# Performance work log

Measured on AMD Instinct MI355X. Metric: run time of the kernel, lower is better.

## Reference

```python
import jax, jax.numpy as jnp
import numpy as np

STRIDES = (8.0, 16.0, 32.0)
REG_MAX = 7
TOP_K = 100          # top_k_n: max per class and max total
NMS_PRE = 1000       # hardcoded prefilter in get_bboxes
IOU_THRES = 0.5      # literal passed to combined_non_max_suppression
BOX_SCORE = 0.3
IMG_SIZE = (640.0, 640.0)


def _centers(h, w, stride):
    # row-major (h, w) flatten, points stored as (y, x)
    y = (jnp.arange(h, dtype=jnp.float32) + 0.5) * stride
    x = (jnp.arange(w, dtype=jnp.float32) + 0.5) * stride
    return jnp.stack([jnp.repeat(y, w), jnp.tile(x, h)], axis=-1)  # [h*w, 2]


def _distribution(bbox_pred, stride):
    # softmax over reg_max+1 bins -> expected distance, scaled by stride
    b = bbox_pred.shape[0]
    p = jax.nn.softmax(bbox_pred.reshape(b, -1, REG_MAX + 1), axis=-1)
    ln = jnp.arange(REG_MAX + 1, dtype=jnp.float32)
    d = jnp.einsum('bnk,k->bn', p, ln).reshape(b, -1, 4)
    return d * stride


def _process_level(cls_score, bbox_pred, stride):
    b, h, w, c = cls_score.shape
    scores = jax.nn.sigmoid(cls_score.reshape(b, h * w, c))
    dist = _distribution(bbox_pred, stride)                     # [b, hw, 4]
    pts = jnp.broadcast_to(_centers(h, w, stride)[None], (b, h * w, 2))
    if h * w > NMS_PRE:  # static shape check, mirrors TF graph specialization
        max_scores = jnp.max(scores, axis=-1)                   # [b, hw]
        _, topk = jax.lax.top_k(max_scores, NMS_PRE)            # [b, NMS_PRE]
        scores = jnp.take_along_axis(scores, topk[..., None], axis=1)
        dist = jnp.take_along_axis(dist, topk[..., None], axis=1)
        pts = jnp.take_along_axis(pts, topk[..., None], axis=1)
    # distance2bbox with clipping to model input shape
    y1 = jnp.clip(pts[..., 0] - dist[..., 0], 0.0, IMG_SIZE[0])
    x1 = jnp.clip(pts[..., 1] - dist[..., 1], 0.0, IMG_SIZE[1])
    y2 = jnp.clip(pts[..., 0] + dist[..., 2], 0.0, IMG_SIZE[0])
    x2 = jnp.clip(pts[..., 1] + dist[..., 3], 0.0, IMG_SIZE[1])
    return jnp.stack([y1, x1, y2, x2], axis=-1), scores


def _iou_1_vs_n(box, boxes):
    yy1 = jnp.maximum(box[0], boxes[:, 0])
    xx1 = jnp.maximum(box[1], boxes[:, 1])
    yy2 = jnp.minimum(box[2], boxes[:, 2])
    xx2 = jnp.minimum(box[3], boxes[:, 3])
    inter = jnp.maximum(yy2 - yy1, 0.0) * jnp.maximum(xx2 - xx1, 0.0)
    a1 = (box[2] - box[0]) * (box[3] - box[1])
    a2 = (boxes[:, 2] - boxes[:, 0]) * (boxes[:, 3] - boxes[:, 1])
    return inter / (a1 + a2 - inter + 1e-9)


def _nms_single(boxes, scores):
    # greedy NMS, fixed TOP_K iterations; boxes [N,4], scores [N]
    def step(s, _):
        i = jnp.argmax(s)
        sc = s[i]
        suppress = _iou_1_vs_n(boxes[i], boxes) > IOU_THRES
        s = jnp.where(suppress, -jnp.inf, s)
        s = s.at[i].set(-jnp.inf)
        return s, (i, sc)
    _, (idx, sel) = jax.lax.scan(step, scores, None, length=TOP_K)
    return idx, sel  # [TOP_K] each


def _combined_nms(boxes, scores):
    # per-class NMS then global top-K, emulating tf.image.combined_non_max_suppression
    n, c = scores.shape
    idx, sel = jax.vmap(_nms_single, in_axes=(None, 1))(boxes, scores)  # [C, K]
    sel_boxes = boxes[idx]                                              # [C, K, 4]
    cls = jnp.broadcast_to(jnp.arange(c, dtype=jnp.float32)[:, None], (c, TOP_K))
    flat_s = sel.reshape(-1)
    flat_s = jnp.where(jnp.isfinite(flat_s), flat_s, -1.0)
    top_s, top_i = jax.lax.top_k(flat_s, TOP_K)
    out_boxes = sel_boxes.reshape(-1, 4)[top_i]
    out_cls = cls.reshape(-1)[top_i]
    ok = top_s > -1.0
    out_s = jnp.where(ok, top_s, 0.0)
    out_boxes = jnp.where(ok[:, None], out_boxes, 0.0)
    out_cls = jnp.where(ok, out_cls, 0.0)
    return out_boxes, out_s, out_cls


def setup_inputs() -> dict:
    key = jax.random.key(0)
    ks = jax.random.split(key, 7)
    b, c = 16, 20
    inp = {}
    for i, hw in enumerate((80, 40, 20)):
        inp[f'cls_score_{i}'] = jax.random.normal(ks[i], (b, hw, hw, c), dtype=jnp.float32)
        inp[f'bbox_pred_{i}'] = jax.random.normal(ks[3 + i], (b, hw, hw, 4 * (REG_MAX + 1)), dtype=jnp.float32)
    inp['origin_shapes'] = jax.random.uniform(ks[6], (b, 2), dtype=jnp.float32) * 1280.0
    return inp


def reference(cls_score_0, cls_score_1, cls_score_2,
              bbox_pred_0, bbox_pred_1, bbox_pred_2, origin_shapes):
    cls_scores = (cls_score_0, cls_score_1, cls_score_2)
    bbox_preds = (bbox_pred_0, bbox_pred_1, bbox_pred_2)
    mlvl_b, mlvl_s = [], []
    for cs, bp, st in zip(cls_scores, bbox_preds, STRIDES):
        bb, sc = _process_level(cs, bp, st)
        mlvl_b.append(bb)
        mlvl_s.append(sc)
    boxes = jnp.concatenate(mlvl_b, axis=1)    # [B, 2400, 4]
    scores = jnp.concatenate(mlvl_s, axis=1)   # [B, 2400, C]
    nb, ns, nc = jax.vmap(_combined_nms)(boxes, scores)
    out = jnp.concatenate([nb, ns[..., None], nc[..., None]], axis=-1)  # [B, K, 6]
    mask = (ns > BOX_SCORE).astype(out.dtype)
    return out * mask[..., None]
```

## Files before the change

### kernel.cpp

```cpp
#include <hip/hip_runtime.h>
#include <math.h>

#define BATCH 16
#define NCLS 20
#define TOPK 100
#define NPRE 1000
#define NTOT 2400
#define NBINS 8
#define N0 6400
#define N1 1600
#define SSEL 256

#define MID05 0.50000002980232238769531250

__device__ __forceinline__ unsigned int orderable(float x) {
    unsigned int u = __float_as_uint(x);
    return (u & 0x80000000u) ? ~u : (u | 0x80000000u);
}
__device__ __forceinline__ float unorderable(unsigned int k) {
    return __uint_as_float((k & 0x80000000u) ? (k ^ 0x80000000u) : ~k);
}

__device__ __forceinline__ void radix_pass_scan(
        const unsigned int* hist, unsigned int* s_prefix, unsigned int* s_kk,
        unsigned int prefix, unsigned int kk, int t) {
    if (t < 64) {
        uint4 h = *(const uint4*)&hist[t * 4];
        unsigned int s3 = h.w;
        unsigned int s2 = h.z + s3;
        unsigned int s1 = h.y + s2;
        unsigned int s0 = h.x + s1;
        unsigned int S = s0;
        #pragma unroll
        for (int off = 1; off < 64; off <<= 1) {
            unsigned int o = __shfl_down(S, off);
            S += (t + off < 64) ? o : 0u;
        }
        unsigned int Sgt = S - s0;
        unsigned int F0 = s0 + Sgt, F1 = s1 + Sgt, F2 = s2 + Sgt, F3 = s3 + Sgt;
        if (F0 >= kk && F1 < kk)  { *s_prefix = (prefix << 8) | (unsigned int)(t * 4 + 0); *s_kk = kk - F1; }
        if (F1 >= kk && F2 < kk)  { *s_prefix = (prefix << 8) | (unsigned int)(t * 4 + 1); *s_kk = kk - F2; }
        if (F2 >= kk && F3 < kk)  { *s_prefix = (prefix << 8) | (unsigned int)(t * 4 + 2); *s_kk = kk - F3; }
        if (F3 >= kk && Sgt < kk) { *s_prefix = (prefix << 8) | (unsigned int)(t * 4 + 3); *s_kk = kk - Sgt; }
    }
}

__device__ __forceinline__ unsigned long long bmerge_shfl(
        unsigned long long v, int t, int k2, int jmax) {
    for (int j2 = jmax; j2 > 0; j2 >>= 1) {
        unsigned long long o = __shfl_xor(v, j2);
        bool km = (((t & k2) == 0) == ((t & j2) != 0));
        v = km ? (v > o ? v : o) : (v < o ? v : o);
    }
    return v;
}

__global__ __launch_bounds__(1024) void select_keys_kernel(
        const float* __restrict__ cls0, const float* __restrict__ cls1,
        int* __restrict__ sel_idx, int* __restrict__ cnt) {
    int bid = blockIdx.x;
    int b = bid >> 1;
    int lvl = bid & 1;
    int n = (lvl == 0) ? N0 : N1;
    const float* cls = (lvl == 0 ? cls0 : cls1) + (size_t)b * (size_t)n * NCLS;

    __shared__ unsigned int skey[N0];
    __shared__ __align__(16) unsigned int hist[256];
    __shared__ int eq[256];
    __shared__ unsigned int s_prefix, s_kk, s_cnt, s_eqcnt;
    int t = threadIdx.x;

    if (bid == 0 && t < BATCH) cnt[t] = 0;

    for (int a = t; a < n; a += 1024) {
        const float4* p4 = (const float4*)(cls + (size_t)a * NCLS);
        float m = -INFINITY;
        #pragma unroll
        for (int q = 0; q < 5; ++q) {
            float4 v = p4[q];
            m = fmaxf(m, fmaxf(fmaxf(v.x, v.y), fmaxf(v.z, v.w)));
        }
        skey[a] = orderable(m);
    }
    if (t == 0) { s_kk = NPRE; s_prefix = 0u; s_cnt = 0u; s_eqcnt = 0u; }
    __syncthreads();

    for (int pass = 0; pass < 4; ++pass) {
        int shift = 24 - 8 * pass;
        unsigned int prefix = s_prefix, kk = s_kk;
        if (t < 256) hist[t] = 0u;
        __syncthreads();
        for (int a = t; a < n; a += 1024) {
            unsigned int u = skey[a];
            if (pass == 0 || (u >> (shift + 8)) == prefix)
                atomicAdd(&hist[(u >> shift) & 255u], 1u);
        }
        __syncthreads();
        radix_pass_scan(hist, &s_prefix, &s_kk, prefix, kk, t);
        __syncthreads();
    }

    unsigned int T = s_prefix;
    int* out = sel_idx + b * 2000 + lvl * 1000;
    for (int a = t; a < n; a += 1024) {
        unsigned int u = skey[a];
        if (u > T) {
            unsigned int pos = atomicAdd(&s_cnt, 1u);
            out[pos] = a;
        } else if (u == T) {
            unsigned int p = atomicAdd(&s_eqcnt, 1u);
            if (p < 256u) eq[p] = a;
        }
    }
    __syncthreads();
    if (t == 0) {
        unsigned int pos = s_cnt;
        unsigned int rem = s_kk;
        unsigned int cnt2 = s_eqcnt;
        if (cnt2 <= 256u) {
            for (unsigned int i = 1; i < cnt2; ++i) {
                int key = eq[i]; int j2 = (int)i - 1;
                while (j2 >= 0 && eq[j2] > key) { eq[j2 + 1] = eq[j2]; --j2; }
                eq[j2 + 1] = key;
            }
            for (unsigned int i = 0; i < rem; ++i) out[pos + i] = eq[i];
        } else {
            for (int a = 0; a < n && rem > 0u; ++a)
                if (skey[a] == T) { out[pos++] = a; --rem; }
        }
    }
}

__global__ __launch_bounds__(256) void decode_kernel(
        const float* __restrict__ cls0, const float* __restrict__ cls1, const float* __restrict__ cls2,
        const float* __restrict__ bb0,  const float* __restrict__ bb1,  const float* __restrict__ bb2,
        const int* __restrict__ sel_idx,
        float* __restrict__ boxes_all, float* __restrict__ scores_t) {
    int tg = blockIdx.x * blockDim.x + threadIdx.x;
    if (tg >= BATCH * NTOT) return;
    int b = tg / NTOT, j = tg % NTOT;

    const float* cls; const float* bb; int a, w; float stride;
    if (j < 1000) {
        a = sel_idx[b * 2000 + j]; w = 80; stride = 8.f;
        cls = cls0 + ((size_t)b * N0 + a) * NCLS;
        bb  = bb0  + ((size_t)b * N0 + a) * 32;
    } else if (j < 2000) {
        a = sel_idx[b * 2000 + j]; w = 40; stride = 16.f;
        cls = cls1 + ((size_t)b * N1 + a) * NCLS;
        bb  = bb1  + ((size_t)b * N1 + a) * 32;
    } else {
        a = j - 2000; w = 20; stride = 32.f;
        cls = cls2 + ((size_t)b * 400 + a) * NCLS;
        bb  = bb2  + ((size_t)b * 400 + a) * 32;
    }

    float cl[20];
    {
        const float4* c4 = (const float4*)cls;
        #pragma unroll
        for (int q = 0; q < 5; ++q) *(float4*)&cl[q * 4] = c4[q];
    }
    float bl[32];
    {
        const float4* b4 = (const float4*)bb;
        #pragma unroll
        for (int q = 0; q < 8; ++q) *(float4*)&bl[q * 4] = b4[q];
    }

    #pragma unroll
    for (int c = 0; c < NCLS; ++c)
        scores_t[((size_t)b * NCLS + c) * NTOT + j] = 1.f / (1.f + expf(-cl[c]));

    float d[4];
    #pragma unroll
    for (int s = 0; s < 4; ++s) {
        const float* l = &bl[s * NBINS];
        float m = l[0];
        #pragma unroll
        for (int k = 1; k < NBINS; ++k) m = fmaxf(m, l[k]);
        float e[NBINS], sum = 0.f;
        #pragma unroll
        for (int k = 0; k < NBINS; ++k) { e[k] = expf(l[k] - m); sum += e[k]; }
        float acc = 0.f;
        #pragma unroll
        for (int k = 0; k < NBINS; ++k) acc += (e[k] / sum) * (float)k;
        d[s] = acc * stride;
    }
    float cy = ((float)(a / w) + 0.5f) * stride;
    float cx = ((float)(a % w) + 0.5f) * stride;
    float* bx = boxes_all + ((size_t)b * NTOT + j) * 4;
    bx[0] = fminf(fmaxf(cy - d[0], 0.f), 640.f);
    bx[1] = fminf(fmaxf(cx - d[1], 0.f), 640.f);
    bx[2] = fminf(fmaxf(cy + d[2], 0.f), 640.f);
    bx[3] = fminf(fmaxf(cx + d[3], 0.f), 640.f);
}

__global__ __launch_bounds__(256) void class_nms_kernel(
        const float* __restrict__ boxes_all, const float* __restrict__ scores_t,
        float* __restrict__ nms_score, int* __restrict__ nms_idx,
        int* __restrict__ cnt, float* __restrict__ outbuf) {
    int blk = blockIdx.x;
    int b = blk / NCLS;
    int t = threadIdx.x;

    __shared__ unsigned int skey[NTOT];
    __shared__ __align__(16) unsigned int hist[256];
    __shared__ int eq[128];
    __shared__ unsigned int s_prefix, s_kk, s_cnt, s_eqcnt;
    __shared__ unsigned long long sorted[SSEL];
    __shared__ float4 abox[TOPK];
    __shared__ float4 cbox[64];
    __shared__ int s_outPos;
    __shared__ unsigned long long s_m;
    __shared__ int s_last;

    const float*  ssrc = scores_t + (size_t)blk * NTOT;
    const float4* bsrc = (const float4*)boxes_all + (size_t)b * NTOT;
    float* osc = nms_score + (size_t)blk * TOPK;
    int*   oid = nms_idx   + (size_t)blk * TOPK;

    for (int j = t; j < NTOT; j += 256) skey[j] = orderable(ssrc[j]);
    if (t == 0) { s_kk = SSEL; s_prefix = 0u; s_cnt = 0u; s_eqcnt = 0u; s_outPos = 0; }
    __syncthreads();

    for (int pass = 0; pass < 4; ++pass) {
        int shift = 24 - 8 * pass;
        unsigned int prefix = s_prefix, kk = s_kk;
        hist[t] = 0u;
        __syncthreads();
        for (int j = t; j < NTOT; j += 256) {
            unsigned int u = skey[j];
            if (pass == 0 || (u >> (shift + 8)) == prefix)
                atomicAdd(&hist[(u >> shift) & 255u], 1u);
        }
        __syncthreads();
        radix_pass_scan(hist, &s_prefix, &s_kk, prefix, kk, t);
        __syncthreads();
    }

    unsigned int T = s_prefix;
    for (int j = t; j < NTOT; j += 256) {
        unsigned int u = skey[j];
        if (u > T) {
            unsigned int pos = atomicAdd(&s_cnt, 1u);
            sorted[pos] = ((unsigned long long)u << 32) | (unsigned int)~j;
        } else if (u == T) {
            unsigned int p = atomicAdd(&s_eqcnt, 1u);
            if (p < 128u) eq[p] = j;
        }
    }
    __syncthreads();
    if (t == 0) {
        unsigned int pos = s_cnt;
        unsigned int rem = s_kk;
        unsigned int cnt2 = s_eqcnt;
        if (cnt2 <= 128u) {
            for (unsigned int i = 1; i < cnt2; ++i) {
                int key = eq[i]; int j2 = (int)i - 1;
                while (j2 >= 0 && eq[j2] > key) { eq[j2 + 1] = eq[j2]; --j2; }
                eq[j2 + 1] = key;
            }
            for (unsigned int i = 0; i < rem; ++i)
                sorted[pos + i] = ((unsigned long long)T << 32) | (unsigned int)~eq[i];
        } else {
            for (int j = 0; j < NTOT && rem > 0u; ++j)
                if (skey[j] == T) {
                    sorted[pos++] = ((unsigned long long)T << 32) | (unsigned int)~j;
                    --rem;
                }
        }
    }
    __syncthreads();

    {
        unsigned long long v = sorted[t];
        #pragma unroll
        for (int k2 = 2; k2 <= 64; k2 <<= 1)
            v = bmerge_shfl(v, t, k2, k2 >> 1);
        sorted[t] = v;
        __syncthreads();
        {
            unsigned long long o = sorted[t ^ 64];
            bool km = (((t & 128) == 0) == ((t & 64) != 0));
            v = km ? (v > o ? v : o) : (v < o ? v : o);
            v = bmerge_shfl(v, t, 128, 32);
        }
        __syncthreads();
        sorted[t] = v;
        __syncthreads();
        {
            unsigned long long o = sorted[t ^ 128];
            bool km = ((t & 128) != 0);
            v = km ? (v > o ? v : o) : (v < o ? v : o);
        }
        __syncthreads();
        sorted[t] = v;
        __syncthreads();
        {
            unsigned long long o = sorted[t ^ 64];
            bool km = ((t & 64) != 0);
            v = km ? (v > o ? v : o) : (v < o ? v : o);
            v = bmerge_shfl(v, t, 256, 32);
        }
        __syncthreads();
        sorted[t] = v;
        __syncthreads();
    }

    if (t < 64) {
        int lane = t;
        int outPos = 0;
        for (int chunk = 0; chunk < SSEL / 64 && outPos < TOPK; ++chunk) {
            unsigned long long key = sorted[SSEL - 1 - (chunk * 64 + lane)];
            unsigned int j = ~(unsigned int)key;
            float sc = unorderable((unsigned int)(key >> 32));
            float4 bj = bsrc[j];
            cbox[lane] = bj;
            float amine = (bj.z - bj.x) * (bj.w - bj.y);

            bool sup = false;
            for (int t2 = 0; t2 < outPos; ++t2) {
                float4 wb = abox[t2];
                float a1 = (wb.z - wb.x) * (wb.w - wb.y);
                float yy1 = fmaxf(wb.x, bj.x);
                float xx1 = fmaxf(wb.y, bj.y);
                float yy2 = fminf(wb.z, bj.z);
                float xx2 = fminf(wb.w, bj.w);
                float inter = fmaxf(yy2 - yy1, 0.f) * fmaxf(xx2 - xx1, 0.f);
                float denom = a1 + amine - inter + 1e-9f;
                sup = sup || ((double)inter > MID05 * (double)denom);
            }

            unsigned long long supmask = 0ull;
            #pragma unroll 8
            for (int j2 = 0; j2 < 64; ++j2) {
                float4 wb = cbox[j2];
                float a1 = (wb.z - wb.x) * (wb.w - wb.y);
                float yy1 = fmaxf(wb.x, bj.x);
                float xx1 = fmaxf(wb.y, bj.y);
                float yy2 = fminf(wb.z, bj.z);
                float xx2 = fminf(wb.w, bj.w);
                float inter = fmaxf(yy2 - yy1, 0.f) * fmaxf(xx2 - xx1, 0.f);
                float denom = a1 + amine - inter + 1e-9f;
                bool s2 = ((double)inter > MID05 * (double)denom);
                if (s2 && j2 < lane) supmask |= (1ull << j2);
            }

            unsigned long long cand = __ballot(!sup);
            unsigned long long accbits = 0ull;
            while (cand) {
                int i = __builtin_ctzll(cand);
                accbits |= (1ull << i);
                cand &= ~(1ull << i);
                unsigned long long row = __ballot((supmask >> i) & 1ull);
                cand &= ~row;
            }

            int nAcc = (int)__builtin_popcountll(accbits);
            int avail = TOPK - outPos;
            bool mine = (accbits >> lane) & 1ull;
            int myrank = (int)__builtin_popcountll(accbits & ((1ull << lane) - 1ull));
            if (mine && myrank < avail) {
                int pos = outPos + myrank;
                osc[pos] = sc;
                oid[pos] = (int)j;
                abox[pos] = bj;
            }
            outPos += (nAcc < avail) ? nAcc : avail;
            __builtin_amdgcn_s_waitcnt(0);
        }
        if (lane == 0) s_outPos = outPos;
    }
    __syncthreads();

    int outPos = s_outPos;
    if (outPos < TOPK) {
        if (t < SSEL) skey[~(unsigned int)sorted[t]] = 0u;
        __syncthreads();
        for (int j = t; j < NTOT; j += 256) {
            unsigned int u = skey[j];
            if (!u) continue;
            float4 bj = bsrc[j];
            float amine = (bj.z - bj.x) * (bj.w - bj.y);
            bool sup = false;
            for (int t2 = 0; t2 < outPos; ++t2) {
                float4 wb = abox[t2];
                float a1 = (wb.z - wb.x) * (wb.w - wb.y);
                float yy1 = fmaxf(wb.x, bj.x);
                float xx1 = fmaxf(wb.y, bj.y);
                float yy2 = fminf(wb.z, bj.z);
                float xx2 = fminf(wb.w, bj.w);
                float inter = fmaxf(yy2 - yy1, 0.f) * fmaxf(xx2 - xx1, 0.f);
                float denom = a1 + amine - inter + 1e-9f;
                sup = sup || ((double)inter > MID05 * (double)denom);
            }
            if (sup) skey[j] = 0u;
        }
        __syncthreads();
        while (outPos < TOPK) {
            if (t == 0) s_m = 0ull;
            __syncthreads();
            unsigned long long loc = 0ull;
            for (int j = t; j < NTOT; j += 256) {
                unsigned int u = skey[j];
                if (u) {
                    unsigned long long kk = ((unsigned long long)u << 32) | (unsigned int)~j;
                    loc = (kk > loc) ? kk : loc;
                }
            }
            atomicMax(&s_m, loc);
            __syncthreads();
            unsigned long long m = s_m;
            if ((long long)m >= 0) break;
            unsigned int wi = ~(unsigned int)m;
            float4 wb = bsrc[wi];
            if (t == 0) {
                osc[outPos] = unorderable((unsigned int)(m >> 32));
                oid[outPos] = (int)wi;
                skey[wi] = 0u;
            }
            __syncthreads();
            float a1 = (wb.z - wb.x) * (wb.w - wb.y);
            for (int j = t; j < NTOT; j += 256) {
                unsigned int u = skey[j];
                if (!u) continue;
                float4 bj = bsrc[j];
                float yy1 = fmaxf(wb.x, bj.x);
                float xx1 = fmaxf(wb.y, bj.y);
                float yy2 = fminf(wb.z, bj.z);
                float xx2 = fminf(wb.w, bj.w);
                float inter = fmaxf(yy2 - yy1, 0.f) * fmaxf(xx2 - xx1, 0.f);
                float a2 = (bj.z - bj.x) * (bj.w - bj.y);
                float denom = a1 + a2 - inter + 1e-9f;
                if ((double)inter > MID05 * (double)denom) skey[j] = 0u;
            }
            ++outPos;
            __syncthreads();
        }
    }

    for (int k2 = outPos + t; k2 < TOPK; k2 += 256) { osc[k2] = -INFINITY; oid[k2] = 0; }

    __syncthreads();
    if (t == 0) {
        __threadfence();
        int old = atomicAdd(&cnt[b], 1);
        s_last = (old == NCLS - 1) ? 1 : 0;
        if (s_last) __threadfence();
    }
    __syncthreads();
    if (!s_last) return;

    for (int f = t; f < 2000; f += 256) {
        float s = nms_score[(size_t)b * 2000 + f];
        float v = isfinite(s) ? s : -1.0f;
        skey[f] = orderable(v);
    }
    if (t == 0) { s_kk = TOPK; s_prefix = 0u; s_cnt = 0u; s_eqcnt = 0u; }
    if (t < 128) sorted[t] = 0ull;
    __syncthreads();

    for (int pass = 0; pass < 4; ++pass) {
        int shift = 24 - 8 * pass;
        unsigned int prefix = s_prefix, kk = s_kk;
        hist[t] = 0u;
        __syncthreads();
        for (int f = t; f < 2000; f += 256) {
            unsigned int u = skey[f];
            if (pass == 0 || (u >> (shift + 8)) == prefix)
                atomicAdd(&hist[(u >> shift) & 255u], 1u);
        }
        __syncthreads();
        radix_pass_scan(hist, &s_prefix, &s_kk, prefix, kk, t);
        __syncthreads();
    }

    unsigned int Tf = s_prefix;
    for (int f = t; f < 2000; f += 256) {
        unsigned int u = skey[f];
        if (u > Tf) {
            unsigned int pos = atomicAdd(&s_cnt, 1u);
            sorted[pos] = ((unsigned long long)u << 32) | (unsigned int)~f;
        } else if (u == Tf) {
            unsigned int p = atomicAdd(&s_eqcnt, 1u);
            if (p < 128u) eq[p] = f;
        }
    }
    __syncthreads();
    if (t == 0) {
        unsigned int pos = s_cnt;
        unsigned int rem = s_kk;
        unsigned int cnt2 = s_eqcnt;
        if (cnt2 <= 128u) {
            for (unsigned int i = 1; i < cnt2; ++i) {
                int key = eq[i]; int j2 = (int)i - 1;
                while (j2 >= 0 && eq[j2] > key) { eq[j2 + 1] = eq[j2]; --j2; }
                eq[j2 + 1] = key;
            }
            for (unsigned int i = 0; i < rem; ++i)
                sorted[pos + i] = ((unsigned long long)Tf << 32) | (unsigned int)~eq[i];
        } else {
            for (int f = 0; f < 2000 && rem > 0u; ++f)
                if (skey[f] == Tf) {
                    sorted[pos++] = ((unsigned long long)Tf << 32) | (unsigned int)~f;
                    --rem;
                }
        }
    }
    __syncthreads();

    {
        unsigned long long v = (t < 128) ? sorted[t] : 0ull;
        if (t < 128) {
            #pragma unroll
            for (int k2 = 2; k2 <= 64; k2 <<= 1)
                v = bmerge_shfl(v, t, k2, k2 >> 1);
            sorted[t] = v;
        }
        __syncthreads();
        if (t < 128) {
            unsigned long long o = sorted[t ^ 64];
            bool km = ((t & 64) != 0);
            v = km ? (v > o ? v : o) : (v < o ? v : o);
            v = bmerge_shfl(v, t, 128, 32);
        }
        __syncthreads();
        if (t < 128) sorted[t] = v;
        __syncthreads();
    }

    if (t < TOPK) {
        unsigned long long kk = sorted[127 - t];
        float v = unorderable((unsigned int)(kk >> 32));
        int fi = (int)~(unsigned int)kk;
        float* o = outbuf + ((size_t)b * TOPK + t) * 6;
        if (v > 0.3f) {
            int bidx = nms_idx[(size_t)b * 2000 + fi];
            float4 bxw = ((const float4*)boxes_all)[(size_t)b * NTOT + bidx];
            o[0] = bxw.x; o[1] = bxw.y; o[2] = bxw.z; o[3] = bxw.w;
            o[4] = v; o[5] = (float)(fi / TOPK);
        } else {
            o[0] = 0.f; o[1] = 0.f; o[2] = 0.f; o[3] = 0.f; o[4] = 0.f; o[5] = 0.f;
        }
    }
}

extern "C" void kernel_launch(void* const* d_in, const int* in_sizes, int n_in,
                              void* d_out, int out_size, void* d_ws, size_t ws_size,
                              hipStream_t stream) {
    (void)out_size; (void)ws_size;
    const float* cls[3] = {nullptr, nullptr, nullptr};
    const float* bbx[3] = {nullptr, nullptr, nullptr};
    for (int i = 0; i < n_in; ++i) {
        const float* p = (const float*)d_in[i];
        switch (in_sizes[i]) {
            case 16 * 6400 * 20: cls[0] = p; break;
            case 16 * 6400 * 32: bbx[0] = p; break;
            case 16 * 1600 * 20: cls[1] = p; break;
            case 16 * 1600 * 32: bbx[1] = p; break;
            case 16 *  400 * 20: cls[2] = p; break;
            case 16 *  400 * 32: bbx[2] = p; break;
            default: break;
        }
    }

    char* w = (char*)d_ws;
    int*   sel_idx    = (int*)(w);
    float* boxes_all  = (float*)(w + 131072);
    float* scores_t   = (float*)(w + 745472);
    float* nms_score  = (float*)(w + 3817472);
    int*   nms_idx    = (int*)(w + 3945472);
    int*   cnt        = (int*)(w + 4073472);

    hipLaunchKernelGGL(select_keys_kernel, dim3(32), dim3(1024), 0, stream,
                       cls[0], cls[1], sel_idx, cnt);
    hipLaunchKernelGGL(decode_kernel, dim3((BATCH * NTOT + 255) / 256), dim3(256), 0, stream,
                       cls[0], cls[1], cls[2], bbx[0], bbx[1], bbx[2],
                       sel_idx, boxes_all, scores_t);
    hipLaunchKernelGGL(class_nms_kernel, dim3(BATCH * NCLS), dim3(256), 0, stream,
                       boxes_all, scores_t, nms_score, nms_idx, cnt, (float*)d_out);
}
```

Before: 154.2 us.

## Split key computation into wide kernel and pair two classes per NMS block

The per-anchor max-score key computation moves out of the 32-block select kernel into a separate fully parallel kernel, and the radix select then reads precomputed keys with 256 threads. The class NMS kernel now processes two classes per 512-thread block, which halves the block count and the final-merge counter threshold. The aim is to remove the low-parallelism prologue of select and to amortize the final per-batch merge across fewer blocks. The cost is an extra launch, a global round-trip for the keys, and more shared memory per NMS block, which may reduce occupancy. The fallback NMS loop for classes that do not finish within the sorted prefix now runs serially over both classes using the whole block.

```diff
diff --git a/kernel.cpp b/kernel.cpp
--- a/kernel.cpp
+++ b/kernel.cpp
@@ -23,46 +23,71 @@
 
 __device__ __forceinline__ void radix_pass_scan(
         const unsigned int* hist, unsigned int* s_prefix, unsigned int* s_kk,
-        unsigned int prefix, unsigned int kk, int t) {
-    if (t < 64) {
-        uint4 h = *(const uint4*)&hist[t * 4];
-        unsigned int s3 = h.w;
-        unsigned int s2 = h.z + s3;
-        unsigned int s1 = h.y + s2;
-        unsigned int s0 = h.x + s1;
-        unsigned int S = s0;
-        #pragma unroll
-        for (int off = 1; off < 64; off <<= 1) {
-            unsigned int o = __shfl_down(S, off);
-            S += (t + off < 64) ? o : 0u;
-        }
-        unsigned int Sgt = S - s0;
-        unsigned int F0 = s0 + Sgt, F1 = s1 + Sgt, F2 = s2 + Sgt, F3 = s3 + Sgt;
-        if (F0 >= kk && F1 < kk)  { *s_prefix = (prefix << 8) | (unsigned int)(t * 4 + 0); *s_kk = kk - F1; }
-        if (F1 >= kk && F2 < kk)  { *s_prefix = (prefix << 8) | (unsigned int)(t * 4 + 1); *s_kk = kk - F2; }
-        if (F2 >= kk && F3 < kk)  { *s_prefix = (prefix << 8) | (unsigned int)(t * 4 + 2); *s_kk = kk - F3; }
-        if (F3 >= kk && Sgt < kk) { *s_prefix = (prefix << 8) | (unsigned int)(t * 4 + 3); *s_kk = kk - Sgt; }
-    }
+        unsigned int prefix, unsigned int kk, int lane) {
+    uint4 h = *(const uint4*)&hist[lane * 4];
+    unsigned int s3 = h.w;
+    unsigned int s2 = h.z + s3;
+    unsigned int s1 = h.y + s2;
+    unsigned int s0 = h.x + s1;
+    unsigned int S = s0;
+    #pragma unroll
+    for (int off = 1; off < 64; off <<= 1) {
+        unsigned int o = __shfl_down(S, off);
+        S += (lane + off < 64) ? o : 0u;
+    }
+    unsigned int Sgt = S - s0;
+    unsigned int F0 = s0 + Sgt, F1 = s1 + Sgt, F2 = s2 + Sgt, F3 = s3 + Sgt;
+    if (F0 >= kk && F1 < kk)  { *s_prefix = (prefix << 8) | (unsigned int)(lane * 4 + 0); *s_kk = kk - F1; }
+    if (F1 >= kk && F2 < kk)  { *s_prefix = (prefix << 8) | (unsigned int)(lane * 4 + 1); *s_kk = kk - F2; }
+    if (F2 >= kk && F3 < kk)  { *s_prefix = (prefix << 8) | (unsigned int)(lane * 4 + 2); *s_kk = kk - F3; }
+    if (F3 >= kk && Sgt < kk) { *s_prefix = (prefix << 8) | (unsigned int)(lane * 4 + 3); *s_kk = kk - Sgt; }
 }
 
 __device__ __forceinline__ unsigned long long bmerge_shfl(
-        unsigned long long v, int t, int k2, int jmax) {
+        unsigned long long v, int pos, int k2, int jmax) {
     for (int j2 = jmax; j2 > 0; j2 >>= 1) {
         unsigned long long o = __shfl_xor(v, j2);
-        bool km = (((t & k2) == 0) == ((t & j2) != 0));
+        bool km = (((pos & k2) == 0) == ((pos & j2) != 0));
         v = km ? (v > o ? v : o) : (v < o ? v : o);
     }
     return v;
 }
 
-__global__ __launch_bounds__(1024) void select_keys_kernel(
+__global__ __launch_bounds__(256) void compute_keys_kernel(
         const float* __restrict__ cls0, const float* __restrict__ cls1,
-        int* __restrict__ sel_idx, int* __restrict__ cnt) {
+        unsigned int* __restrict__ keys0, unsigned int* __restrict__ keys1,
+        int* __restrict__ cnt) {
+    int tg = blockIdx.x * 256 + threadIdx.x;
+    if (blockIdx.x == 0 && threadIdx.x < BATCH) cnt[threadIdx.x] = 0;
+    const float* p;
+    unsigned int* dst;
+    if (tg < BATCH * N0) {
+        p = cls0 + (size_t)tg * NCLS;
+        dst = keys0 + tg;
+    } else {
+        int a = tg - BATCH * N0;
+        if (a >= BATCH * N1) return;
+        p = cls1 + (size_t)a * NCLS;
+        dst = keys1 + a;
+    }
+    const float4* p4 = (const float4*)p;
+    float m = -INFINITY;
+    #pragma unroll
+    for (int q = 0; q < 5; ++q) {
+        float4 v = p4[q];
+        m = fmaxf(m, fmaxf(fmaxf(v.x, v.y), fmaxf(v.z, v.w)));
+    }
+    *dst = orderable(m);
+}
+
+__global__ __launch_bounds__(256) void radix_select_kernel(
+        const unsigned int* __restrict__ keys0, const unsigned int* __restrict__ keys1,
+        int* __restrict__ sel_idx) {
     int bid = blockIdx.x;
     int b = bid >> 1;
     int lvl = bid & 1;
     int n = (lvl == 0) ? N0 : N1;
-    const float* cls = (lvl == 0 ? cls0 : cls1) + (size_t)b * (size_t)n * NCLS;
+    const unsigned int* gk = (lvl == 0 ? keys0 : keys1) + (size_t)b * n;
 
     __shared__ unsigned int skey[N0];
     __shared__ __align__(16) unsigned int hist[256];
@@ -70,39 +95,28 @@
     __shared__ unsigned int s_prefix, s_kk, s_cnt, s_eqcnt;
     int t = threadIdx.x;
 
-    if (bid == 0 && t < BATCH) cnt[t] = 0;
-
-    for (int a = t; a < n; a += 1024) {
-        const float4* p4 = (const float4*)(cls + (size_t)a * NCLS);
-        float m = -INFINITY;
-        #pragma unroll
-        for (int q = 0; q < 5; ++q) {
-            float4 v = p4[q];
-            m = fmaxf(m, fmaxf(fmaxf(v.x, v.y), fmaxf(v.z, v.w)));
-        }
-        skey[a] = orderable(m);
-    }
+    for (int a = t; a < n; a += 256) skey[a] = gk[a];
     if (t == 0) { s_kk = NPRE; s_prefix = 0u; s_cnt = 0u; s_eqcnt = 0u; }
     __syncthreads();
 
     for (int pass = 0; pass < 4; ++pass) {
         int shift = 24 - 8 * pass;
         unsigned int prefix = s_prefix, kk = s_kk;
-        if (t < 256) hist[t] = 0u;
-        __syncthreads();
-        for (int a = t; a < n; a += 1024) {
+        hist[t] = 0u;
+        __syncthreads();
+        for (int a = t; a < n; a += 256) {
             unsigned int u = skey[a];
             if (pass == 0 || (u >> (shift + 8)) == prefix)
                 atomicAdd(&hist[(u >> shift) & 255u], 1u);
         }
         __syncthreads();
-        radix_pass_scan(hist, &s_prefix, &s_kk, prefix, kk, t);
+        if (t < 64) radix_pass_scan(hist, &s_prefix, &s_kk, prefix, kk, t);
         __syncthreads();
     }
 
     unsigned int T = s_prefix;
     int* out = sel_idx + b * 2000 + lvl * 1000;
-    for (int a = t; a < n; a += 1024) {
+    for (int a = t; a < n; a += 256) {
         unsigned int u = skey[a];
         if (u > T) {
             unsigned int pos = atomicAdd(&s_cnt, 1u);
@@ -196,77 +210,82 @@
     bx[3] = fminf(fmaxf(cx + d[3], 0.f), 640.f);
 }
 
-__global__ __launch_bounds__(256) void class_nms_kernel(
+__global__ __launch_bounds__(512) void class_nms_kernel(
         const float* __restrict__ boxes_all, const float* __restrict__ scores_t,
         float* __restrict__ nms_score, int* __restrict__ nms_idx,
         int* __restrict__ cnt, float* __restrict__ outbuf) {
     int blk = blockIdx.x;
-    int b = blk / NCLS;
+    int b = blk / 10;
+    int pair = blk % 10;
     int t = threadIdx.x;
-
-    __shared__ unsigned int skey[NTOT];
-    __shared__ __align__(16) unsigned int hist[256];
-    __shared__ int eq[128];
-    __shared__ unsigned int s_prefix, s_kk, s_cnt, s_eqcnt;
-    __shared__ unsigned long long sorted[SSEL];
-    __shared__ float4 abox[TOPK];
-    __shared__ float4 cbox[64];
-    __shared__ int s_outPos;
-    __shared__ unsigned long long s_m;
+    int ci = t >> 8;
+    int tl = t & 255;
+    int c = pair * 2 + ci;
+
+    __shared__ unsigned int skey[2][NTOT];
+    __shared__ __align__(16) unsigned int hist[2][256];
+    __shared__ int eq[2][128];
+    __shared__ unsigned int s_prefix[2], s_kk[2], s_cnt[2], s_eqcnt[2];
+    __shared__ unsigned long long sorted[2][SSEL];
+    __shared__ float4 abox[2][TOPK];
+    __shared__ float4 cbox[2][64];
+    __shared__ int s_outPos[2];
+    __shared__ unsigned long long s_m[2];
     __shared__ int s_last;
 
-    const float*  ssrc = scores_t + (size_t)blk * NTOT;
+    const float*  ssrc = scores_t + ((size_t)b * NCLS + c) * NTOT;
     const float4* bsrc = (const float4*)boxes_all + (size_t)b * NTOT;
-    float* osc = nms_score + (size_t)blk * TOPK;
-    int*   oid = nms_idx   + (size_t)blk * TOPK;
-
-    for (int j = t; j < NTOT; j += 256) skey[j] = orderable(ssrc[j]);
-    if (t == 0) { s_kk = SSEL; s_prefix = 0u; s_cnt = 0u; s_eqcnt = 0u; s_outPos = 0; }
+    float* osc = nms_score + ((size_t)b * NCLS + c) * TOPK;
+    int*   oid = nms_idx   + ((size_t)b * NCLS + c) * TOPK;
+
+    for (int j = tl; j < NTOT; j += 256) skey[ci][j] = orderable(ssrc[j]);
+    if (tl == 0) { s_kk[ci] = SSEL; s_prefix[ci] = 0u; s_cnt[ci] = 0u; s_eqcnt[ci] = 0u; s_outPos[ci] = 0; }
     __syncthreads();
 
     for (int pass = 0; pass < 4; ++pass) {
         int shift = 24 - 8 * pass;
-        unsigned int prefix = s_prefix, kk = s_kk;
-        hist[t] = 0u;
-        __syncthreads();
-        for (int j = t; j < NTOT; j += 256) {
-            unsigned int u = skey[j];
+        unsigned int prefix = s_prefix[ci], kk = s_kk[ci];
+        hist[ci][tl] = 0u;
+        __syncthreads();
+        for (int j = tl; j < NTOT; j += 256) {
+            unsigned int u = skey[ci][j];
             if (pass == 0 || (u >> (shift + 8)) == prefix)
-                atomicAdd(&hist[(u >> shift) & 255u], 1u);
-        }
-        __syncthreads();
-        radix_pass_scan(hist, &s_prefix, &s_kk, prefix, kk, t);
-        __syncthreads();
-    }
-
-    unsigned int T = s_prefix;
-    for (int j = t; j < NTOT; j += 256) {
-        unsigned int u = skey[j];
+                atomicAdd(&hist[ci][(u >> shift) & 255u], 1u);
+        }
+        __syncthreads();
+        if (tl < 64)
+            radix_pass_scan(hist[ci], &s_prefix[ci], &s_kk[ci], prefix, kk, tl);
+        __syncthreads();
+    }
+
+    unsigned int T = s_prefix[ci];
+    for (int j = tl; j < NTOT; j += 256) {
+        unsigned int u = skey[ci][j];
         if (u > T) {
-            unsigned int pos = atomicAdd(&s_cnt, 1u);
-            sorted[pos] = ((unsigned long long)u << 32) | (unsigned int)~j;
+            unsigned int pos = atomicAdd(&s_cnt[ci], 1u);
+            sorted[ci][pos] = ((unsigned long long)u << 32) | (unsigned int)~j;
         } else if (u == T) {
-            unsigned int p = atomicAdd(&s_eqcnt, 1u);
-            if (p < 128u) eq[p] = j;
-        }
-    }
-    __syncthreads();
-    if (t == 0) {
-        unsigned int pos = s_cnt;
-        unsigned int rem = s_kk;
-        unsigned int cnt2 = s_eqcnt;
+            unsigned int p = atomicAdd(&s_eqcnt[ci], 1u);
+            if (p < 128u) eq[ci][p] = j;
+        }
+    }
+    __syncthreads();
+    if (tl == 0) {
+        unsigned int pos = s_cnt[ci];
+        unsigned int rem = s_kk[ci];
+        unsigned int cnt2 = s_eqcnt[ci];
         if (cnt2 <= 128u) {
             for (unsigned int i = 1; i < cnt2; ++i) {
-                int key = eq[i]; int j2 = (int)i - 1;
-                while (j2 >= 0 && eq[j2] > key) { eq[j2 + 1] = eq[j2]; --j2; }
-                eq[j2 + 1] = key;
+                int key = eq[ci][i]; int j2 = (int)i - 1;
+                while (j2 >= 0 && eq[ci][j2] > key) { eq[ci][j2 + 1] = eq[ci][j2]; --j2; }
+                eq[ci][j2 + 1] = key;
             }
             for (unsigned int i = 0; i < rem; ++i)
-                sorted[pos + i] = ((unsigned long long)T << 32) | (unsigned int)~eq[i];
+                sorted[ci][pos + i] = ((unsigned long long)T << 32) | (unsigned int)~eq[ci][i];
         } else {
             for (int j = 0; j < NTOT && rem > 0u; ++j)
-                if (skey[j] == T) {
-                    sorted[pos++] = ((unsigned long long)T << 32) | (unsigned int)~j;
+                if (skey[ci][j] == T) {
+                    sorted[ci][pos++] = ((unsigned long long)T << 32) | (unsigned int)~j;
                     --rem;
                 }
         }
@@ -274,54 +293,54 @@
     __syncthreads();
 
     {
-        unsigned long long v = sorted[t];
+        unsigned long long v = sorted[ci][tl];
         #pragma unroll
         for (int k2 = 2; k2 <= 64; k2 <<= 1)
-            v = bmerge_shfl(v, t, k2, k2 >> 1);
-        sorted[t] = v;
+            v = bmerge_shfl(v, tl, k2, k2 >> 1);
+        sorted[ci][tl] = v;
         __syncthreads();
         {
-            unsigned long long o = sorted[t ^ 64];
-            bool km = (((t & 128) == 0) == ((t & 64) != 0));
+            unsigned long long o = sorted[ci][tl ^ 64];
+            bool km = (((tl & 128) == 0) == ((tl & 64) != 0));
             v = km ? (v > o ? v : o) : (v < o ? v : o);
-            v = bmerge_shfl(v, t, 128, 32);
-        }
-        __syncthreads();
-        sorted[t] = v;
+            v = bmerge_shfl(v, tl, 128, 32);
+        }
+        __syncthreads();
+        sorted[ci][tl] = v;
         __syncthreads();
         {
-            unsigned long long o = sorted[t ^ 128];
-            bool km = ((t & 128) != 0);
+            unsigned long long o = sorted[ci][tl ^ 128];
+            bool km = ((tl & 128) != 0);
             v = km ? (v > o ? v : o) : (v < o ? v : o);
         }
         __syncthreads();
-        sorted[t] = v;
+        sorted[ci][tl] = v;
         __syncthreads();
         {
-            unsigned long long o = sorted[t ^ 64];
-            bool km = ((t & 64) != 0);
+            unsigned long long o = sorted[ci][tl ^ 64];
+            bool km = ((tl & 64) != 0);
             v = km ? (v > o ? v : o) : (v < o ? v : o);
-            v = bmerge_shfl(v, t, 256, 32);
-        }
-        __syncthreads();
-        sorted[t] = v;
-        __syncthreads();
-    }
-
-    if (t < 64) {
-        int lane = t;
+            v = bmerge_shfl(v, tl, 256, 32);
+        }
+        __syncthreads();
+        sorted[ci][tl] = v;
+        __syncthreads();
+    }
+
+    if (tl < 64) {
+        int lane = tl;
         int outPos = 0;
         for (int chunk = 0; chunk < SSEL / 64 && outPos < TOPK; ++chunk) {
-            unsigned long long key = sorted[SSEL - 1 - (chunk * 64 + lane)];
+            unsigned long long key = sorted[ci][SSEL - 1 - (chunk * 64 + lane)];
             unsigned int j = ~(unsigned int)key;
             float sc = unorderable((unsigned int)(key >> 32));
             float4 bj = bsrc[j];
-            cbox[lane] = bj;
+            cbox[ci][lane] = bj;
             float amine = (bj.z - bj.x) * (bj.w - bj.y);
 
             bool sup = false;
             for (int t2 = 0; t2 < outPos; ++t2) {
-                float4 wb = abox[t2];
+                float4 wb = abox[ci][t2];
                 float a1 = (wb.z - wb.x) * (wb.w - wb.y);
                 float yy1 = fmaxf(wb.x, bj.x);
                 float xx1 = fmaxf(wb.y, bj.y);
@@ -335,7 +354,7 @@
             unsigned long long supmask = 0ull;
             #pragma unroll 8
             for (int j2 = 0; j2 < 64; ++j2) {
-                float4 wb = cbox[j2];
+                float4 wb = cbox[ci][j2];
                 float a1 = (wb.z - wb.x) * (wb.w - wb.y);
                 float yy1 = fmaxf(wb.x, bj.x);
                 float xx1 = fmaxf(wb.y, bj.y);
@@ -365,145 +384,155 @@
                 int pos = outPos + myrank;
                 osc[pos] = sc;
                 oid[pos] = (int)j;
-                abox[pos] = bj;
+                abox[ci][pos] = bj;
             }
             outPos += (nAcc < avail) ? nAcc : avail;
             __builtin_amdgcn_s_waitcnt(0);
         }
-        if (lane == 0) s_outPos = outPos;
-    }
-    __syncthreads();
-
-    int outPos = s_outPos;
-    if (outPos < TOPK) {
-        if (t < SSEL) skey[~(unsigned int)sorted[t]] = 0u;
-        __syncthreads();
-        for (int j = t; j < NTOT; j += 256) {
-            unsigned int u = skey[j];
-            if (!u) continue;
-            float4 bj = bsrc[j];
-            float amine = (bj.z - bj.x) * (bj.w - bj.y);
-            bool sup = false;
-            for (int t2 = 0; t2 < outPos; ++t2) {
-                float4 wb = abox[t2];
-                float a1 = (wb.z - wb.x) * (wb.w - wb.y);
-                float yy1 = fmaxf(wb.x, bj.x);
-                float xx1 = fmaxf(wb.y, bj.y);
-                float yy2 = fminf(wb.z, bj.z);
-                float xx2 = fminf(wb.w, bj.w);
-                float inter = fmaxf(yy2 - yy1, 0.f) * fmaxf(xx2 - xx1, 0.f);
-                float denom = a1 + amine - inter + 1e-9f;
-                sup = sup || ((double)inter > MID05 * (double)denom);
-            }
-            if (sup) skey[j] = 0u;
-        }
-        __syncthreads();
-        while (outPos < TOPK) {
-            if (t == 0) s_m = 0ull;
+        if (lane == 0) s_outPos[ci] = outPos;
+    }
+    __syncthreads();
+
+    for (int ci2 = 0; ci2 < 2; ++ci2) {
+        int outPos = s_outPos[ci2];
+        if (outPos < TOPK) {
+            int c2 = pair * 2 + ci2;
+            float* osc2 = nms_score + ((size_t)b * NCLS + c2) * TOPK;
+            int*   oid2 = nms_idx   + ((size_t)b * NCLS + c2) * TOPK;
+            if (t < SSEL) skey[ci2][~(unsigned int)sorted[ci2][t]] = 0u;
             __syncthreads();
-            unsigned long long loc = 0ull;
-            for (int j = t; j < NTOT; j += 256) {
-                unsigned int u = skey[j];
-                if (u) {
-                    unsigned long long kk = ((unsigned long long)u << 32) | (unsigned int)~j;
-                    loc = (kk > loc) ? kk : loc;
-                }
-            }
-            atomicMax(&s_m, loc);
-            __syncthreads();
-            unsigned long long m = s_m;
-            if ((long long)m >= 0) break;
-            unsigned int wi = ~(unsigned int)m;
-            float4 wb = bsrc[wi];
-            if (t == 0) {
-                osc[outPos] = unorderable((unsigned int)(m >> 32));
-                oid[outPos] = (int)wi;
-                skey[wi] = 0u;
-            }
-            __syncthreads();
-            float a1 = (wb.z - wb.x) * (wb.w - wb.y);
-            for (int j = t; j < NTOT; j += 256) {
-                unsigned int u = skey[j];
+            for (int j = t; j < NTOT; j += 512) {
+                unsigned int u = skey[ci2][j];
                 if (!u) continue;
                 float4 bj = bsrc[j];
-                float yy1 = fmaxf(wb.x, bj.x);
-                float xx1 = fmaxf(wb.y, bj.y);
-                float yy2 = fminf(wb.z, bj.z);
-                float xx2 = fminf(wb.w, bj.w);
-                float inter = fmaxf(yy2 - yy1, 0.f) * fmaxf(xx2 - xx1, 0.f);
-                float a2 = (bj.z - bj.x) * (bj.w - bj.y);
-                float denom = a1 + a2 - inter + 1e-9f;
-                if ((double)inter > MID05 * (double)denom) skey[j] = 0u;
-            }
-            ++outPos;
+                float amine = (bj.z - bj.x) * (bj.w - bj.y);
+                bool sup = false;
+                for (int t2 = 0; t2 < outPos; ++t2) {
+                    float4 wb = abox[ci2][t2];
+                    float a1 = (wb.z - wb.x) * (wb.w - wb.y);
+                    float yy1 = fmaxf(wb.x, bj.x);
+                    float xx1 = fmaxf(wb.y, bj.y);
+                    float yy2 = fminf(wb.z, bj.z);
+                    float xx2 = fminf(wb.w, bj.w);
+                    float inter = fmaxf(yy2 - yy1, 0.f) * fmaxf(xx2 - xx1, 0.f);
+                    float denom = a1 + amine - inter + 1e-9f;
+                    sup = sup || ((double)inter > MID05 * (double)denom);
+                }
+                if (sup) skey[ci2][j] = 0u;
+            }
             __syncthreads();
-        }
-    }
-
-    for (int k2 = outPos + t; k2 < TOPK; k2 += 256) { osc[k2] = -INFINITY; oid[k2] = 0; }
+            while (outPos < TOPK) {
+                if (t == 0) s_m[ci2] = 0ull;
+                __syncthreads();
+                unsigned long long loc = 0ull;
+                for (int j = t; j < NTOT; j += 512) {
+                    unsigned int u = skey[ci2][j];
+                    if (u) {
+                        unsigned long long kk = ((unsigned long long)u << 32) | (unsigned int)~j;
+                        loc = (kk > loc) ? kk : loc;
+                    }
+                }
+                atomicMax(&s_m[ci2], loc);
+                __syncthreads();
+                unsigned long long m = s_m[ci2];
+                if ((long long)m >= 0) break;
+                unsigned int wi = ~(unsigned int)m;
+                float4 wb = bsrc[wi];
+                if (t == 0) {
+                    osc2[outPos] = unorderable((unsigned int)(m >> 32));
+                    oid2[outPos] = (int)wi;
+                    skey[ci2][wi] = 0u;
+                }
+                __syncthreads();
+                float a1 = (wb.z - wb.x) * (wb.w - wb.y);
+                for (int j = t; j < NTOT; j += 512) {
+                    unsigned int u = skey[ci2][j];
+                    if (!u) continue;
+                    float4 bj = bsrc[j];
+                    float yy1 = fmaxf(wb.x, bj.x);
+                    float xx1 = fmaxf(wb.y, bj.y);
+                    float yy2 = fminf(wb.z, bj.z);
+                    float xx2 = fminf(wb.w, bj.w);
+                    float inter = fmaxf(yy2 - yy1, 0.f) * fmaxf(xx2 - xx1, 0.f);
+                    float a2 = (bj.z - bj.x) * (bj.w - bj.y);
+                    float denom = a1 + a2 - inter + 1e-9f;
+                    if ((double)inter > MID05 * (double)denom) skey[ci2][j] = 0u;
+                }
+                ++outPos;
+                __syncthreads();
+            }
+            if (t == 0) s_outPos[ci2] = outPos;
+            __syncthreads();
+        }
+    }
+
+    {
+        int op = s_outPos[ci];
+        for (int k2 = op + tl; k2 < TOPK; k2 += 256) { osc[k2] = -INFINITY; oid[k2] = 0; }
+    }
 
     __syncthreads();
     if (t == 0) {
         __threadfence();
         int old = atomicAdd(&cnt[b], 1);
-        s_last = (old == NCLS - 1) ? 1 : 0;
+        s_last = (old == 9) ? 1 : 0;
         if (s_last) __threadfence();
     }
     __syncthreads();
     if (!s_last) return;
 
-    for (int f = t; f < 2000; f += 256) {
+    for (int f = t; f < 2000; f += 512) {
         float s = nms_score[(size_t)b * 2000 + f];
         float v = isfinite(s) ? s : -1.0f;
-        skey[f] = orderable(v);
-    }
-    if (t == 0) { s_kk = TOPK; s_prefix = 0u; s_cnt = 0u; s_eqcnt = 0u; }
-    if (t < 128) sorted[t] = 0ull;
+        skey[0][f] = orderable(v);
+    }
+    if (t == 0) { s_kk[0] = TOPK; s_prefix[0] = 0u; s_cnt[0] = 0u; s_eqcnt[0] = 0u; }
+    if (t < 128) sorted[0][t] = 0ull;
     __syncthreads();
 
     for (int pass = 0; pass < 4; ++pass) {
         int shift = 24 - 8 * pass;
-        unsigned int prefix = s_prefix, kk = s_kk;
-        hist[t] = 0u;
-        __syncthreads();
-        for (int f = t; f < 2000; f += 256) {
-            unsigned int u = skey[f];
+        unsigned int prefix = s_prefix[0], kk = s_kk[0];
+        if (t < 256) hist[0][t] = 0u;
+        __syncthreads();
+        for (int f = t; f < 2000; f += 512) {
+            unsigned int u = skey[0][f];
             if (pass == 0 || (u >> (shift + 8)) == prefix)
-                atomicAdd(&hist[(u >> shift) & 255u], 1u);
-        }
-        __syncthreads();
-        radix_pass_scan(hist, &s_prefix, &s_kk, prefix, kk, t);
-        __syncthreads();
-    }
-
-    unsigned int Tf = s_prefix;
-    for (int f = t; f < 2000; f += 256) {
-        unsigned int u = skey[f];
+                atomicAdd(&hist[0][(u >> shift) & 255u], 1u);
+        }
+        __syncthreads();
+        if (t < 64) radix_pass_scan(hist[0], &s_prefix[0], &s_kk[0], prefix, kk, t);
+        __syncthreads();
+    }
+
+    unsigned int Tf = s_prefix[0];
+    for (int f = t; f < 2000; f += 512) {
+        unsigned int u = skey[0][f];
         if (u > Tf) {
-            unsigned int pos = atomicAdd(&s_cnt, 1u);
-            sorted[pos] = ((unsigned long long)u << 32) | (unsigned int)~f;
+            unsigned int pos = atomicAdd(&s_cnt[0], 1u);
+            sorted[0][pos] = ((unsigned long long)u << 32) | (unsigned int)~f;
         } else if (u == Tf) {
-            unsigned int p = atomicAdd(&s_eqcnt, 1u);
-            if (p < 128u) eq[p] = f;
+            unsigned int p = atomicAdd(&s_eqcnt[0], 1u);
+            if (p < 128u) eq[0][p] = f;
         }
     }
     __syncthreads();
     if (t == 0) {
-        unsigned int pos = s_cnt;
-        unsigned int rem = s_kk;
-        unsigned int cnt2 = s_eqcnt;
+        unsigned int pos = s_cnt[0];
+        unsigned int rem = s_kk[0];
+        unsigned int cnt2 = s_eqcnt[0];
         if (cnt2 <= 128u) {
             for (unsigned int i = 1; i < cnt2; ++i) {
-                int key = eq[i]; int j2 = (int)i - 1;
-                while (j2 >= 0 && eq[j2] > key) { eq[j2 + 1] = eq[j2]; --j2; }
-                eq[j2 + 1] = key;
+                int key = eq[0][i]; int j2 = (int)i - 1;
+                while (j2 >= 0 && eq[0][j2] > key) { eq[0][j2 + 1] = eq[0][j2]; --j2; }
+                eq[0][j2 + 1] = key;
             }
             for (unsigned int i = 0; i < rem; ++i)
-                sorted[pos + i] = ((unsigned long long)Tf << 32) | (unsigned int)~eq[i];
+                sorted[0][pos + i] = ((unsigned long long)Tf << 32) | (unsigned int)~eq[0][i];
         } else {
             for (int f = 0; f < 2000 && rem > 0u; ++f)
-                if (skey[f] == Tf) {
-                    sorted[pos++] = ((unsigned long long)Tf << 32) | (unsigned int)~f;
+                if (skey[0][f] == Tf) {
+                    sorted[0][pos++] = ((unsigned long long)Tf << 32) | (unsigned int)~f;
                     --rem;
                 }
         }
@@ -511,27 +540,27 @@
     __syncthreads();
 
     {
-        unsigned long long v = (t < 128) ? sorted[t] : 0ull;
+        unsigned long long v = (t < 128) ? sorted[0][t] : 0ull;
         if (t < 128) {
             #pragma unroll
             for (int k2 = 2; k2 <= 64; k2 <<= 1)
                 v = bmerge_shfl(v, t, k2, k2 >> 1);
-            sorted[t] = v;
+            sorted[0][t] = v;
         }
         __syncthreads();
         if (t < 128) {
-            unsigned long long o = sorted[t ^ 64];
+            unsigned long long o = sorted[0][t ^ 64];
             bool km = ((t & 64) != 0);
             v = km ? (v > o ? v : o) : (v < o ? v : o);
             v = bmerge_shfl(v, t, 128, 32);
         }
         __syncthreads();
-        if (t < 128) sorted[t] = v;
+        if (t < 128) sorted[0][t] = v;
         __syncthreads();
     }
 
     if (t < TOPK) {
-        unsigned long long kk = sorted[127 - t];
+        unsigned long long kk = sorted[0][127 - t];
         float v = unorderable((unsigned int)(kk >> 32));
         int fi = (int)~(unsigned int)kk;
         float* o = outbuf + ((size_t)b * TOPK + t) * 6;
@@ -569,15 +598,19 @@
     int*   sel_idx    = (int*)(w);
     float* boxes_all  = (float*)(w + 131072);
     float* scores_t   = (float*)(w + 745472);
+    unsigned int* keys0 = (unsigned int*)(w + 745472);
+    unsigned int* keys1 = (unsigned int*)(w + 745472 + 409600);
     float* nms_score  = (float*)(w + 3817472);
     int*   nms_idx    = (int*)(w + 3945472);
     int*   cnt        = (int*)(w + 4073472);
 
-    hipLaunchKernelGGL(select_keys_kernel, dim3(32), dim3(1024), 0, stream,
-                       cls[0], cls[1], sel_idx, cnt);
+    hipLaunchKernelGGL(compute_keys_kernel, dim3((BATCH * (N0 + N1) + 255) / 256), dim3(256), 0, stream,
+                       cls[0], cls[1], keys0, keys1, cnt);
+    hipLaunchKernelGGL(radix_select_kernel, dim3(32), dim3(256), 0, stream,
+                       keys0, keys1, sel_idx);
     hipLaunchKernelGGL(decode_kernel, dim3((BATCH * NTOT + 255) / 256), dim3(256), 0, stream,
                        cls[0], cls[1], cls[2], bbx[0], bbx[1], bbx[2],
                        sel_idx, boxes_all, scores_t);
-    hipLaunchKernelGGL(class_nms_kernel, dim3(BATCH * NCLS), dim3(256), 0, stream,
+    hipLaunchKernelGGL(class_nms_kernel, dim3(BATCH * NCLS / 2), dim3(512), 0, stream,
                        boxes_all, scores_t, nms_score, nms_idx, cnt, (float*)d_out);
 }
```

After: 155.4 us. About the same (+0.8%).
